# Kernel optimization log

Measured on AMD Instinct MI355X. Metric: run time of the kernel, lower is better.

The kernel has to match this reference:

```python
import jax, jax.numpy as jnp
import numpy as np
from jax import lax

P = 16        # patch spatial size (C = 3 * P * P = 768)
CH = 3        # channels per patch
H = 8         # num attention heads
EPS_BN = 1e-3 # keras BatchNormalization default epsilon
EPS_LN = 1e-3 # keras LayerNormalization default epsilon


def _layernorm(x, g, b):
    mu = jnp.mean(x, axis=-1, keepdims=True)
    var = jnp.mean(jnp.square(x - mu), axis=-1, keepdims=True)
    return (x - mu) * lax.rsqrt(var + EPS_LN) * g + b


def setup_inputs() -> dict:
    key = jax.random.key(0)
    ks = jax.random.split(key, 8)
    B, N, C, DFF = 8, 1024, 768, 3072
    s = 0.02
    return {
        "encoded_patches": jax.random.normal(ks[0], (B, N, C), jnp.float32),
        "qconv_w": jax.random.normal(ks[1], (3, 3, CH, CH), jnp.float32) * 0.2,
        "reatten_w": jax.random.normal(ks[2], (H, H), jnp.float32) * 0.3,
        "reatten_b": jnp.zeros((H,), jnp.float32),
        "bn_gamma": jnp.ones((H,), jnp.float32),
        "bn_beta": jnp.zeros((H,), jnp.float32),
        "proj_w": jax.random.normal(ks[3], (C, C), jnp.float32) * s,
        "proj_b": jnp.zeros((C,), jnp.float32),
        "ffn_w1": jax.random.normal(ks[4], (C, DFF), jnp.float32) * s,
        "ffn_b1": jnp.zeros((DFF,), jnp.float32),
        "ffn_w2": jax.random.normal(ks[5], (DFF, C), jnp.float32) * s,
        "ffn_b2": jnp.zeros((C,), jnp.float32),
        "ln1_g": jnp.ones((C,), jnp.float32),
        "ln1_b": jnp.zeros((C,), jnp.float32),
        "ln2_g": jnp.ones((C,), jnp.float32),
        "ln2_b": jnp.zeros((C,), jnp.float32),
    }


def reference(encoded_patches, qconv_w, reatten_w, reatten_b, bn_gamma, bn_beta,
              proj_w, proj_b, ffn_w1, ffn_b1, ffn_w2, ffn_b2,
              ln1_g, ln1_b, ln2_g, ln2_b):
    B, N, C = encoded_patches.shape
    hd = C // H
    scale = jnp.float32(hd) ** -0.5

    # create_queries: unflatten [B,N,C] -> [B*N,P,P,CH], 3x3 'same' conv,
    # flatten back and split heads -> [B,H,N,hd]. Source uses qconv2d for
    # q, k AND v, so q == k == v; compute once.
    y = encoded_patches.reshape(B * N, P, P, CH)
    y = lax.conv_general_dilated(y, qconv_w, (1, 1), 'SAME',
                                 dimension_numbers=('NHWC', 'HWIO', 'NHWC'))
    q = y.reshape(B, N, H, hd).transpose(0, 2, 1, 3)  # [B,H,N,hd]
    k = q
    v = q

    # attention scores + softmax: [B,H,N,N]
    attn = jax.nn.softmax(jnp.einsum('bhnd,bhmd->bhnm', q, k) * scale, axis=-1)

    # re-attention: 1x1 conv mixing heads + BatchNorm (inference: mean=0, var=1)
    attn = jnp.einsum('bhnm,gh->bgnm', attn, reatten_w) + reatten_b[None, :, None, None]
    bn_s = bn_gamma * lax.rsqrt(jnp.float32(1.0) + EPS_BN)
    attn = attn * bn_s[None, :, None, None] + bn_beta[None, :, None, None]
    # reatten_scale = 1.0 (transform_scale=False)

    x = jnp.einsum('bhnm,bhmd->bhnd', attn, v)        # [B,H,N,hd]
    x = x.transpose(0, 2, 1, 3).reshape(B, N, C)
    x = x @ proj_w + proj_b

    x = x + encoded_patches          # residual
    x = _layernorm(x, ln1_g, ln1_b)  # LN1

    h = jax.nn.gelu(x @ ffn_w1 + ffn_b1, approximate=False)
    x = (h @ ffn_w2 + ffn_b2) + x    # FFN + residual
    x = _layernorm(x, ln2_g, ln2_b)  # LN2
    return x
```

## Files before the change

kernel.cpp:

```cpp
#include <hip/hip_runtime.h>
#include <hip/hip_bf16.h>
#include <math.h>

#define B_ 8
#define N_ 1024
#define C_ 768
#define H_ 8
#define HD_ 96
#define DFF_ 3072
#define SC2_ 0.14724454f
#define SH2_ 11.5415602f

typedef __attribute__((ext_vector_type(8))) short bf16x8;
typedef __attribute__((ext_vector_type(4))) float f32x4;
typedef __attribute__((ext_vector_type(4))) short sh4;

__device__ __forceinline__ short f2bf(float f){
  __hip_bfloat16 h = __float2bfloat16(f);
  return __builtin_bit_cast(short, h);
}
__device__ __forceinline__ float bf2f(short s){
  unsigned u = ((unsigned)(unsigned short)s) << 16;
  return __builtin_bit_cast(float, u);
}
#define MFMA16(a,b,c) __builtin_amdgcn_mfma_f32_16x16x32_bf16((a),(b),(c),0,0,0)

__device__ __forceinline__ void gload16(const void* g, void* l){
  __builtin_amdgcn_global_load_lds((const __attribute__((address_space(1))) unsigned int*)g,
                                   (__attribute__((address_space(3))) unsigned int*)l, 16, 0, 0);
}

__global__ void conv_q_kernel(const float* __restrict__ x, const float* __restrict__ w,
                              short* __restrict__ qb){
  int p = blockIdx.x;
  int t = threadIdx.x;
  __shared__ float xs[768];
  __shared__ float ws[81];
  const float* xp = x + (size_t)p * 768;
  xs[t] = xp[t]; xs[t+256] = xp[t+256]; xs[t+512] = xp[t+512];
  if (t < 81) ws[t] = w[t];
  __syncthreads();
  int i = t >> 4, j = t & 15;
  float a0=0.f, a1=0.f, a2=0.f;
  #pragma unroll
  for (int di=0; di<3; ++di){
    int ii = i + di - 1;
    if (ii < 0 || ii > 15) continue;
    #pragma unroll
    for (int dj=0; dj<3; ++dj){
      int jj = j + dj - 1;
      if (jj < 0 || jj > 15) continue;
      const float* cell = &xs[(ii*16+jj)*3];
      const float* wp = &ws[(di*3+dj)*9];
      #pragma unroll
      for (int ci=0; ci<3; ++ci){
        float xv = cell[ci];
        a0 += xv * wp[ci*3+0];
        a1 += xv * wp[ci*3+1];
        a2 += xv * wp[ci*3+2];
      }
    }
  }
  short* qp = qb + (size_t)p*768 + t*3;
  qp[0]=f2bf(a0); qp[1]=f2bf(a1); qp[2]=f2bf(a2);
}

__global__ void vt_kernel(const short* __restrict__ in, short* __restrict__ out){
  __shared__ short tile[32][33];
  int b = blockIdx.z;
  int c0 = blockIdx.x*32, n0 = blockIdx.y*32;
  int t = threadIdx.x;
  const short* ib = in + (size_t)b*N_*C_;
  short* ob = out + (size_t)b*C_*N_;
  #pragma unroll
  for (int i=0;i<4;i++){
    int idx = i*256+t; int r = idx>>5, cc = idx&31;
    tile[r][cc] = ib[(size_t)(n0+r)*C_ + c0+cc];
  }
  __syncthreads();
  #pragma unroll
  for (int i=0;i<4;i++){
    int idx = i*256+t; int r = idx>>5, cc = idx&31;
    ob[(size_t)(c0+r)*N_ + n0+cc] = tile[cc][r];
  }
}

__global__ void wtrans_kernel(const float* __restrict__ in, short* __restrict__ out,
                              int K, int Nn){
  __shared__ float tile[32][33];
  int n0 = blockIdx.x*32, k0 = blockIdx.y*32;
  int t = threadIdx.x;
  #pragma unroll
  for (int i=0;i<4;i++){
    int idx=i*256+t; int r=idx>>5, cc=idx&31;
    tile[r][cc] = in[(size_t)(k0+r)*Nn + n0+cc];
  }
  __syncthreads();
  #pragma unroll
  for (int i=0;i<4;i++){
    int idx=i*256+t; int r=idx>>5, cc=idx&31;
    out[(size_t)(n0+r)*K + k0+cc] = f2bf(tile[cc][r]);
  }
}

__global__ __launch_bounds__(256, 2)
void qkexp_kernel(const short* __restrict__ qb, short* __restrict__ Pt,
                  float* __restrict__ lsums, int b0)
{
  __shared__ short Ks[64*104];
  int bid = blockIdx.x;
  int bhl = bid >> 4, nt = bid & 15;
  int b = b0 + (bhl >> 3), h = bhl & 7;
  int n0 = nt*64;
  int t = threadIdx.x, w = t>>6, l = t&63, lg = l>>4, lr = l&15;
  const short* qbase = qb + (size_t)b*N_*C_;

  bf16x8 qf[3];
  #pragma unroll
  for (int kc=0;kc<3;++kc)
    qf[kc] = *(const bf16x8*)(qbase + (size_t)(n0 + w*16 + lr)*C_ + h*HD_ + kc*32 + lg*8);

  bf16x8 kreg[3];
  #pragma unroll
  for (int i=0;i<3;++i){
    int id = i*256+t; int r = id/12, c = id%12;
    kreg[i] = *(const bf16x8*)(qbase + (size_t)r*C_ + h*HD_ + c*8);
  }

  float lsum = 0.f;
  short* prow = Pt + ((size_t)bhl*1024 + n0 + w*16 + lr)*1024;

  for (int mt=0; mt<16; ++mt){
    int m0 = mt*64;
    __syncthreads();
    #pragma unroll
    for (int i=0;i<3;++i){
      int id = i*256+t; int r = id/12, c = id%12;
      *(bf16x8*)&Ks[r*104 + c*8] = kreg[i];
    }
    __syncthreads();
    if (mt < 15){
      int m1 = m0 + 64;
      #pragma unroll
      for (int i=0;i<3;++i){
        int id = i*256+t; int r = id/12, c = id%12;
        kreg[i] = *(const bf16x8*)(qbase + (size_t)(m1+r)*C_ + h*HD_ + c*8);
      }
    }
    #pragma unroll
    for (int s=0;s<4;++s){
      f32x4 sacc = (f32x4){0.f,0.f,0.f,0.f};
      bf16x8 kf[3];
      #pragma unroll
      for (int kc=0;kc<3;++kc)
        kf[kc] = *(const bf16x8*)&Ks[(s*16+lr)*104 + kc*32 + lg*8];
      #pragma unroll
      for (int kc=0;kc<3;++kc)
        sacc = MFMA16(kf[kc], qf[kc], sacc);
      sh4 pv;
      #pragma unroll
      for (int r=0;r<4;++r){
        float e = exp2f(sacc[r]*SC2_ - SH2_);
        lsum += e;
        pv[r] = f2bf(e);
      }
      *(sh4*)&prow[m0 + s*16 + lg*4] = pv;
    }
  }
  lsum += __shfl_xor(lsum, 16);
  lsum += __shfl_xor(lsum, 32);
  if (l < 16) lsums[(size_t)bhl*1024 + n0 + w*16 + l] = lsum;
}

__device__ __forceinline__ void load_mix(const short* __restrict__ Pt, int b_local,
                                         int n0, int m0, int t,
                                         const float wl[4][8], float cw, bf16x8 amc[4]){
  #pragma unroll
  for (int i=0;i<4;++i){
    int r = i*32 + (t>>3), mo = t&7;
    const short* p0 = Pt + ((size_t)(b_local*8)*1024 + (size_t)(n0+r))*1024 + m0 + mo*8;
    float pm[8];
    #pragma unroll
    for (int j=0;j<8;++j) pm[j] = cw;
    #pragma unroll
    for (int h=0;h<8;++h){
      bf16x8 ph = *(const bf16x8*)(p0 + (size_t)h*1024*1024);
      #pragma unroll
      for (int j=0;j<8;++j) pm[j] += wl[i][h]*bf2f(ph[j]);
    }
    #pragma unroll
    for (int j=0;j<8;++j) amc[i][j] = f2bf(pm[j]);
  }
}

__global__ __launch_bounds__(256, 2)
void mixpv_kernel(const short* __restrict__ Pt, const float* __restrict__ lsums,
                  const short* __restrict__ vt, const float* __restrict__ rw,
                  const float* __restrict__ rb, const float* __restrict__ bng,
                  const float* __restrict__ bnb, short* __restrict__ out, int b0)
{
  __shared__ short Am[128*68];
  int bid = blockIdx.x;
  int rank = bid>>3;
  int g = rank & 7;
  int p = (bid&7) + ((rank>>3)<<3);
  int b_local = p>>3;
  int n0 = (p&7)*128;
  int b = b0 + b_local;
  int t = threadIdx.x, w = t>>6, l = t&63, lg = l>>4, lr = l&15;

  float bns = bng[g]*rsqrtf(1.001f);
  float cw = rb[g]*bns + bnb[g];
  float wl[4][8];
  #pragma unroll
  for (int i=0;i<4;++i){
    int r = i*32 + (t>>3);
    #pragma unroll
    for (int h=0;h<8;++h)
      wl[i][h] = (rw[g*8+h]*bns) / lsums[(size_t)(b_local*8+h)*1024 + n0 + r];
  }

  f32x4 acc[2][6];
  #pragma unroll
  for (int a=0;a<2;++a)
    #pragma unroll
    for (int nt=0;nt<6;++nt) acc[a][nt] = (f32x4){0.f,0.f,0.f,0.f};

  bf16x8 amc[4];
  load_mix(Pt, b_local, n0, 0, t, wl, cw, amc);
  const short* vbase = vt + (size_t)b*C_*N_ + (size_t)g*HD_*N_;

  for (int mt=0; mt<16; ++mt){
    int m0 = mt*64;
    __syncthreads();
    #pragma unroll
    for (int i=0;i<4;++i){
      int r = i*32 + (t>>3), mo = t&7;
      *(bf16x8*)&Am[r*68 + mo*8] = amc[i];
    }
    __syncthreads();
    if (mt < 15) load_mix(Pt, b_local, n0, m0+64, t, wl, cw, amc);
    #pragma unroll
    for (int kc=0;kc<2;++kc){
      bf16x8 af[2], bfr[6];
      #pragma unroll
      for (int a=0;a<2;++a)
        af[a] = *(const bf16x8*)&Am[(w*32 + a*16 + lr)*68 + kc*32 + lg*8];
      #pragma unroll
      for (int nt=0;nt<6;++nt)
        bfr[nt] = *(const bf16x8*)(vbase + (size_t)(nt*16+lr)*N_ + m0 + kc*32 + lg*8);
      #pragma unroll
      for (int a=0;a<2;++a)
        #pragma unroll
        for (int nt=0;nt<6;++nt)
          acc[a][nt] = MFMA16(af[a], bfr[nt], acc[a][nt]);
    }
  }

  short* obase = out + (size_t)b*N_*C_;
  #pragma unroll
  for (int a=0;a<2;++a)
    #pragma unroll
    for (int nt=0;nt<6;++nt)
      #pragma unroll
      for (int r=0;r<4;++r)
        obase[(size_t)(n0 + w*32 + a*16 + lg*4 + r)*C_ + g*HD_ + nt*16 + lr]
            = f2bf(acc[a][nt][r]);
}

template<int EPI>
__global__ __launch_bounds__(256, 2)
void gemm_bt_kernel(const short* __restrict__ A, const short* __restrict__ Bt,
                    const float* __restrict__ bias, const float* __restrict__ res,
                    float* __restrict__ Of, short* __restrict__ Ob,
                    int M, int Nn, int K)
{
  __shared__ __align__(16) char smem[65536];
  short* Sb = (short*)smem;
  int gm = blockIdx.y*128, gn = blockIdx.x*128;
  int tid = threadIdx.x;
  int w = tid>>6, l = tid&63, lg = l>>4, lr = l&15;
  int wr = w>>1, wc = w&1;
  int srow = l>>3;
  int sg = (l&7) ^ srow;

  const short* Ap = A  + (size_t)(gm + w*8 + srow)*K + sg*8;
  const short* Bp = Bt + (size_t)(gn + w*8 + srow)*K + sg*8;

  f32x4 acc[4][4];
  #pragma unroll
  for (int mt=0;mt<4;++mt)
    #pragma unroll
    for (int nt=0;nt<4;++nt) acc[mt][nt] = (f32x4){0.f,0.f,0.f,0.f};

  int nk = K >> 6;

  auto stage = [&](int tt){
    short* dA = Sb + (tt&1)*16384;
    short* dB = dA + 8192;
    int kb = tt<<6;
    #pragma unroll
    for (int j=0;j<4;++j){
      gload16(Ap + (size_t)j*32*K + kb, dA + (j*32 + w*8)*64);
      gload16(Bp + (size_t)j*32*K + kb, dB + (j*32 + w*8)*64);
    }
  };

  stage(0);
  if (nk > 1) stage(1);

  for (int t=0; t<nk; ++t){
    if (t < nk-1) asm volatile("s_waitcnt vmcnt(8)" ::: "memory");
    else          asm volatile("s_waitcnt vmcnt(0)" ::: "memory");
    __builtin_amdgcn_s_barrier();
    short* CA = Sb + (t&1)*16384;
    short* CB = CA + 8192;
    #pragma unroll
    for (int kc=0;kc<2;++kc){
      bf16x8 af[4], bfr[4];
      #pragma unroll
      for (int mt=0;mt<4;++mt){
        int row = wr*64+mt*16+lr;
        af[mt] = *(const bf16x8*)&CA[row*64 + (((kc*4+lg)^(lr&7))*8)];
      }
      #pragma unroll
      for (int nt=0;nt<4;++nt){
        int row = wc*64+nt*16+lr;
        bfr[nt] = *(const bf16x8*)&CB[row*64 + (((kc*4+lg)^(lr&7))*8)];
      }
      #pragma unroll
      for (int mt=0;mt<4;++mt)
        #pragma unroll
        for (int nt=0;nt<4;++nt)
          acc[mt][nt] = MFMA16(af[mt], bfr[nt], acc[mt][nt]);
    }
    asm volatile("s_waitcnt lgkmcnt(0)" ::: "memory");
    __builtin_amdgcn_sched_barrier(0);
    __builtin_amdgcn_s_barrier();
    if (t+2 < nk) stage(t+2);
  }

  __builtin_amdgcn_s_barrier();
  float* Cl = (float*)smem;
  #pragma unroll
  for (int mt=0;mt<4;++mt)
    #pragma unroll
    for (int nt=0;nt<4;++nt)
      #pragma unroll
      for (int r=0;r<4;++r){
        int row = wr*64 + mt*16 + lg*4 + r;
        int col = wc*64 + nt*16 + lr;
        Cl[row*128 + (col ^ ((row&7)<<2))] = acc[mt][nt][r];
      }
  __syncthreads();
  #pragma unroll
  for (int seg=0; seg<16; ++seg){
    int row = seg*8 + (tid>>5);
    int col = (tid&31)*4;
    int colp = col ^ ((row&7)<<2);
    f32x4 c = *(f32x4*)&Cl[row*128 + colp];
    float4 bi = *(const float4*)&bias[gn+col];
    size_t goff = (size_t)(gm+row)*Nn + gn + col;
    if (EPI == 0){
      float4 rs = *(const float4*)&res[goff];
      float4 o = { c[0]+bi.x+rs.x, c[1]+bi.y+rs.y, c[2]+bi.z+rs.z, c[3]+bi.w+rs.w };
      *(float4*)&Of[goff] = o;
    } else {
      float v0 = c[0]+bi.x, v1 = c[1]+bi.y, v2 = c[2]+bi.z, v3 = c[3]+bi.w;
      v0 = 0.5f*v0*(1.0f + erff(v0*0.70710678118654752f));
      v1 = 0.5f*v1*(1.0f + erff(v1*0.70710678118654752f));
      v2 = 0.5f*v2*(1.0f + erff(v2*0.70710678118654752f));
      v3 = 0.5f*v3*(1.0f + erff(v3*0.70710678118654752f));
      sh4 ob = { f2bf(v0), f2bf(v1), f2bf(v2), f2bf(v3) };
      *(sh4*)&Ob[goff] = ob;
    }
  }
}

template<int WB>
__global__ void ln_kernel(const float* __restrict__ in, const float* __restrict__ gam,
                          const float* __restrict__ bet, float* __restrict__ of,
                          short* __restrict__ ob)
{
  int row = blockIdx.x*4 + (threadIdx.x>>6);
  int l = threadIdx.x & 63;
  const float* ip = in + (size_t)row*C_;
  float v[12];
  #pragma unroll
  for (int i=0;i<3;i++) *(float4*)&v[i*4] = *(const float4*)(ip + i*256 + l*4);
  float s = 0.f;
  #pragma unroll
  for (int i=0;i<12;i++) s += v[i];
  #pragma unroll
  for (int off=1; off<64; off<<=1) s += __shfl_xor(s, off);
  float mu = s * (1.0f/768.0f);
  float q = 0.f;
  #pragma unroll
  for (int i=0;i<12;i++){ float d = v[i]-mu; q += d*d; }
  #pragma unroll
  for (int off=1; off<64; off<<=1) q += __shfl_xor(q, off);
  float rstd = rsqrtf(q*(1.0f/768.0f) + 1e-3f);
  #pragma unroll
  for (int i=0;i<3;i++){
    float4 gv = *(const float4*)(gam + i*256 + l*4);
    float4 bv = *(const float4*)(bet + i*256 + l*4);
    float o0 = (v[i*4+0]-mu)*rstd*gv.x + bv.x;
    float o1 = (v[i*4+1]-mu)*rstd*gv.y + bv.y;
    float o2 = (v[i*4+2]-mu)*rstd*gv.z + bv.z;
    float o3 = (v[i*4+3]-mu)*rstd*gv.w + bv.w;
    float4 ov = {o0,o1,o2,o3};
    *(float4*)(of + (size_t)row*C_ + i*256 + l*4) = ov;
    if (WB){
      sh4 obv = { f2bf(o0), f2bf(o1), f2bf(o2), f2bf(o3) };
      *(sh4*)(ob + (size_t)row*C_ + i*256 + l*4) = obv;
    }
  }
}

extern "C" void kernel_launch(void* const* d_in, const int* in_sizes, int n_in,
                              void* d_out, int out_size, void* d_ws, size_t ws_size,
                              hipStream_t stream)
{
  const float* enc       = (const float*)d_in[0];
  const float* qconv_w   = (const float*)d_in[1];
  const float* reatten_w = (const float*)d_in[2];
  const float* reatten_b = (const float*)d_in[3];
  const float* bn_gamma  = (const float*)d_in[4];
  const float* bn_beta   = (const float*)d_in[5];
  const float* proj_w    = (const float*)d_in[6];
  const float* proj_b    = (const float*)d_in[7];
  const float* ffn_w1    = (const float*)d_in[8];
  const float* ffn_b1    = (const float*)d_in[9];
  const float* ffn_w2    = (const float*)d_in[10];
  const float* ffn_b2    = (const float*)d_in[11];
  const float* ln1_g     = (const float*)d_in[12];
  const float* ln1_b     = (const float*)d_in[13];
  const float* ln2_g     = (const float*)d_in[14];
  const float* ln2_b     = (const float*)d_in[15];
  float* outp = (float*)d_out;

  char* ws = (char*)d_ws;
  short* qbuf  = (short*)(ws);
  short* vtbuf = (short*)(ws + 12582912);
  short* atbuf = (short*)(ws + 25165824);
  short* ptbuf = (short*)(ws + 37748736);
  float* lsums = (float*)(ws + 104857600);
  float* ypre  = (float*)(ws + 37748736);
  float* x1    = (float*)(ws + 62914560);
  short* x1b   = (short*)(ws + 88080384);
  short* hbuf  = (short*)(ws + 100663296);
  short* wpt   = (short*)(ws + 150994944);
  short* w1t   = (short*)(ws + 152174592);
  short* w2t   = (short*)(ws + 156893184);

  conv_q_kernel<<<B_*N_, 256, 0, stream>>>(enc, qconv_w, qbuf);
  vt_kernel<<<dim3(C_/32, N_/32, B_), 256, 0, stream>>>(qbuf, vtbuf);
  wtrans_kernel<<<dim3(C_/32,  C_/32), 256, 0, stream>>>(proj_w, wpt, C_,  C_);
  wtrans_kernel<<<dim3(DFF_/32, C_/32), 256, 0, stream>>>(ffn_w1, w1t, C_,  DFF_);
  wtrans_kernel<<<dim3(C_/32, DFF_/32), 256, 0, stream>>>(ffn_w2, w2t, DFF_, C_);

  for (int half=0; half<2; ++half){
    int b0 = half*4;
    qkexp_kernel<<<512, 256, 0, stream>>>(qbuf, ptbuf, lsums, b0);
    mixpv_kernel<<<256, 256, 0, stream>>>(ptbuf, lsums, vtbuf, reatten_w, reatten_b,
                                          bn_gamma, bn_beta, atbuf, b0);
  }

  gemm_bt_kernel<0><<<dim3(C_/128, (B_*N_)/128), 256, 0, stream>>>(
      atbuf, wpt, proj_b, enc, ypre, nullptr, B_*N_, C_, C_);
  ln_kernel<1><<<(B_*N_)/4, 256, 0, stream>>>(ypre, ln1_g, ln1_b, x1, x1b);
  gemm_bt_kernel<1><<<dim3(DFF_/128, (B_*N_)/128), 256, 0, stream>>>(
      x1b, w1t, ffn_b1, nullptr, nullptr, hbuf, B_*N_, DFF_, C_);
  gemm_bt_kernel<0><<<dim3(C_/128, (B_*N_)/128), 256, 0, stream>>>(
      hbuf, w2t, ffn_b2, x1, ypre, nullptr, B_*N_, C_, DFF_);
  ln_kernel<0><<<(B_*N_)/4, 256, 0, stream>>>(ypre, ln2_g, ln2_b, outp, nullptr);
}
```

Before: 390.3 us.

## Restructure GEMM pipeline, remap blocks across XCDs, add setprio and fast GELU

```diff
diff --git a/kernel.cpp b/kernel.cpp
--- a/kernel.cpp
+++ b/kernel.cpp
@@ -28,6 +28,12 @@
 __device__ __forceinline__ void gload16(const void* g, void* l){
   __builtin_amdgcn_global_load_lds((const __attribute__((address_space(1))) unsigned int*)g,
                                    (__attribute__((address_space(3))) unsigned int*)l, 16, 0, 0);
+}
+
+__device__ __forceinline__ float gelu_fast(float v){
+  float v2 = v*v;
+  float t = v*(2.30206086f + 0.10294103f*v2);
+  return v / (1.0f + exp2f(-t));
 }
 
 __global__ void conv_q_kernel(const float* __restrict__ x, const float* __restrict__ w,
@@ -273,11 +279,13 @@
 void gemm_bt_kernel(const short* __restrict__ A, const short* __restrict__ Bt,
                     const float* __restrict__ bias, const float* __restrict__ res,
                     float* __restrict__ Of, short* __restrict__ Ob,
-                    int M, int Nn, int K)
+                    int M, int Nn, int K, int nxt)
 {
   __shared__ __align__(16) char smem[65536];
   short* Sb = (short*)smem;
-  int gm = blockIdx.y*128, gn = blockIdx.x*128;
+  int cpx = gridDim.x >> 3;
+  int s = (blockIdx.x & 7)*cpx + (blockIdx.x >> 3);
+  int gn = (s % nxt)*128, gm = (s / nxt)*128;
   int tid = threadIdx.x;
   int w = tid>>6, l = tid&63, lg = l>>4, lr = l&15;
   int wr = w>>1, wc = w&1;
@@ -307,12 +315,11 @@
   };
 
   stage(0);
-  if (nk > 1) stage(1);
+  asm volatile("s_waitcnt vmcnt(0)" ::: "memory");
+  __builtin_amdgcn_s_barrier();
 
   for (int t=0; t<nk; ++t){
-    if (t < nk-1) asm volatile("s_waitcnt vmcnt(8)" ::: "memory");
-    else          asm volatile("s_waitcnt vmcnt(0)" ::: "memory");
-    __builtin_amdgcn_s_barrier();
+    if (t+1 < nk) stage(t+1);
     short* CA = Sb + (t&1)*16384;
     short* CB = CA + 8192;
     #pragma unroll
@@ -328,19 +335,18 @@
         int row = wc*64+nt*16+lr;
         bfr[nt] = *(const bf16x8*)&CB[row*64 + (((kc*4+lg)^(lr&7))*8)];
       }
+      __builtin_amdgcn_s_setprio(1);
       #pragma unroll
       for (int mt=0;mt<4;++mt)
         #pragma unroll
         for (int nt=0;nt<4;++nt)
           acc[mt][nt] = MFMA16(af[mt], bfr[nt], acc[mt][nt]);
-    }
-    asm volatile("s_waitcnt lgkmcnt(0)" ::: "memory");
-    __builtin_amdgcn_sched_barrier(0);
+      __builtin_amdgcn_s_setprio(0);
+    }
+    asm volatile("s_waitcnt vmcnt(0)" ::: "memory");
     __builtin_amdgcn_s_barrier();
-    if (t+2 < nk) stage(t+2);
-  }
-
-  __builtin_amdgcn_s_barrier();
+  }
+
   float* Cl = (float*)smem;
   #pragma unroll
   for (int mt=0;mt<4;++mt)
@@ -366,12 +372,8 @@
       float4 o = { c[0]+bi.x+rs.x, c[1]+bi.y+rs.y, c[2]+bi.z+rs.z, c[3]+bi.w+rs.w };
       *(float4*)&Of[goff] = o;
     } else {
-      float v0 = c[0]+bi.x, v1 = c[1]+bi.y, v2 = c[2]+bi.z, v3 = c[3]+bi.w;
-      v0 = 0.5f*v0*(1.0f + erff(v0*0.70710678118654752f));
-      v1 = 0.5f*v1*(1.0f + erff(v1*0.70710678118654752f));
-      v2 = 0.5f*v2*(1.0f + erff(v2*0.70710678118654752f));
-      v3 = 0.5f*v3*(1.0f + erff(v3*0.70710678118654752f));
-      sh4 ob = { f2bf(v0), f2bf(v1), f2bf(v2), f2bf(v3) };
+      sh4 ob = { f2bf(gelu_fast(c[0]+bi.x)), f2bf(gelu_fast(c[1]+bi.y)),
+                 f2bf(gelu_fast(c[2]+bi.z)), f2bf(gelu_fast(c[3]+bi.w)) };
       *(sh4*)&Ob[goff] = ob;
     }
   }
@@ -466,12 +468,12 @@
                                           bn_gamma, bn_beta, atbuf, b0);
   }
 
-  gemm_bt_kernel<0><<<dim3(C_/128, (B_*N_)/128), 256, 0, stream>>>(
-      atbuf, wpt, proj_b, enc, ypre, nullptr, B_*N_, C_, C_);
+  gemm_bt_kernel<0><<<(C_/128)*((B_*N_)/128), 256, 0, stream>>>(
+      atbuf, wpt, proj_b, enc, ypre, nullptr, B_*N_, C_, C_, C_/128);
   ln_kernel<1><<<(B_*N_)/4, 256, 0, stream>>>(ypre, ln1_g, ln1_b, x1, x1b);
-  gemm_bt_kernel<1><<<dim3(DFF_/128, (B_*N_)/128), 256, 0, stream>>>(
-      x1b, w1t, ffn_b1, nullptr, nullptr, hbuf, B_*N_, DFF_, C_);
-  gemm_bt_kernel<0><<<dim3(C_/128, (B_*N_)/128), 256, 0, stream>>>(
-      hbuf, w2t, ffn_b2, x1, ypre, nullptr, B_*N_, C_, DFF_);
+  gemm_bt_kernel<1><<<(DFF_/128)*((B_*N_)/128), 256, 0, stream>>>(
+      x1b, w1t, ffn_b1, nullptr, nullptr, hbuf, B_*N_, DFF_, C_, DFF_/128);
+  gemm_bt_kernel<0><<<(C_/128)*((B_*N_)/128), 256, 0, stream>>>(
+      hbuf, w2t, ffn_b2, x1, ypre, nullptr, B_*N_, C_, DFF_, C_/128);
   ln_kernel<0><<<(B_*N_)/4, 256, 0, stream>>>(ypre, ln2_g, ln2_b, outp, nullptr);
 }
```

Result: faster. 375.0 us (-3.9%).
